# Optimization experiments

Hardware: AMD Instinct MI355X
Metric: run time of the kernel (lower is better)

The kernel has to match this reference:

```python
import jax, jax.numpy as jnp
import numpy as np

NUM_HEADS = 16


def setup_inputs() -> dict:
    key = jax.random.key(0)
    ks = jax.random.split(key, 5)
    B, N, D = 2, 2048, 1024
    scale = 1.0 / np.sqrt(D)  # roughly xavier-ish magnitude for weights
    return {
        "x": jax.random.normal(ks[0], (B, N, D), dtype=jnp.float32),
        "W_query": jax.random.normal(ks[1], (D, D), dtype=jnp.float32) * scale,
        "W_key": jax.random.normal(ks[2], (D, D), dtype=jnp.float32) * scale,
        "W_value": jax.random.normal(ks[3], (D, D), dtype=jnp.float32) * scale,
        "W_output": jax.random.normal(ks[4], (D, D), dtype=jnp.float32) * scale,
    }


def reference(x, W_query, W_key, W_value, W_output):
    # x: [B, N, D]; weights: [D, D]
    B, N, D = x.shape
    H = NUM_HEADS
    hd = D // H

    def mh_embed(W):
        # linear_embedding then split heads: [B, N, D] -> [B, H, N, hd]
        y = jnp.einsum("bnd,de->bne", x, W)
        return y.reshape(B, N, H, hd).transpose(0, 2, 1, 3)

    q = mh_embed(W_query)
    k = mh_embed(W_key)
    v = mh_embed(W_value)

    # NOTE: source scales by token_dim**-0.5 (full model dim), not head_dim
    attn = jnp.einsum("bhnd,bhmd->bhnm", q, k) * (D ** -0.5)
    attn = jax.nn.softmax(attn, axis=-1)
    out = jnp.einsum("bhnm,bhmd->bhnd", attn, v)  # [B, H, N, hd]

    out = out.transpose(0, 2, 1, 3).reshape(B, N, D)  # merge heads
    out = jnp.einsum("bnd,de->bne", out, W_output)
    return out
```

## Files before the change

### kernel.cpp

```cpp
#include <hip/hip_runtime.h>

#define D_MODEL 1024
#define N_TOK   2048
#define NHEAD   16
#define HDIM    64
#define BATCH   2
#define M_TOT   (BATCH*N_TOK)

typedef unsigned short u16;
typedef __bf16 bf16x8 __attribute__((ext_vector_type(8)));
typedef float  f32x4  __attribute__((ext_vector_type(4)));

#define QSCALE 0.04508422002777439f

__device__ __forceinline__ u16 f2bf(float f) {
  union { float f; unsigned u; } v; v.f = f;
  unsigned r = v.u + 0x7fffu + ((v.u >> 16) & 1u);
  return (u16)(r >> 16);
}

__device__ __forceinline__ float bf2f(u16 u) {
  union { unsigned u; float f; } v; v.u = ((unsigned)u) << 16; return v.f;
}

__device__ __forceinline__ unsigned pk2bf(float a, float b) {
#if __has_builtin(__builtin_amdgcn_cvt_pk_bf16_f32)
  typedef __bf16 bf16x2_t __attribute__((ext_vector_type(2)));
  bf16x2_t r = __builtin_amdgcn_cvt_pk_bf16_f32(a, b);
  union { bf16x2_t v; unsigned u; } c; c.v = r; return c.u;
#else
  return (unsigned)f2bf(a) | ((unsigned)f2bf(b) << 16);
#endif
}

__device__ __forceinline__ void gl2lds16(const void* g, void* l) {
  __builtin_amdgcn_global_load_lds(
      (__attribute__((address_space(1))) void*)g,
      (__attribute__((address_space(3))) void*)l, 16, 0, 0);
}

__global__ void prep_kernel(const float* __restrict__ x,
                            const float* __restrict__ s0, const float* __restrict__ s1,
                            const float* __restrict__ s2, const float* __restrict__ s3,
                            u16* __restrict__ xb,
                            u16* __restrict__ d0, u16* __restrict__ d1,
                            u16* __restrict__ d2, u16* __restrict__ d3) {
  const int t = threadIdx.y * 32 + threadIdx.x;
  if (blockIdx.z == 4) {
    int base = (blockIdx.y * 32 + blockIdx.x) * 256 + t;
#pragma unroll
    for (int r = 0; r < 4; ++r) {
      int i = base + r * 262144;
      float4 v = ((const float4*)x)[i];
      ushort4 o;
      o.x = f2bf(v.x); o.y = f2bf(v.y); o.z = f2bf(v.z); o.w = f2bf(v.w);
      ((ushort4*)xb)[i] = o;
    }
    return;
  }
  const float* src; u16* dst;
  switch (blockIdx.z) {
    case 0:  src = s0; dst = d0; break;
    case 1:  src = s1; dst = d1; break;
    case 2:  src = s2; dst = d2; break;
    default: src = s3; dst = d3; break;
  }
  float sc = (blockIdx.z == 0) ? QSCALE : 1.0f;
  __shared__ float tile[32][33];
  int xg = blockIdx.x * 32 + threadIdx.x;
  int ybase = blockIdx.y * 32;
#pragma unroll
  for (int r = 0; r < 4; ++r)
    tile[threadIdx.y + r*8][threadIdx.x] = src[(size_t)(ybase + threadIdx.y + r*8)*D_MODEL + xg];
  __syncthreads();
#pragma unroll
  for (int r = 0; r < 4; ++r)
    dst[(size_t)(blockIdx.x*32 + threadIdx.y + r*8)*D_MODEL + ybase + threadIdx.x] =
        f2bf(tile[threadIdx.x][threadIdx.y + r*8] * sc);
}

__device__ __forceinline__ void gemm_body(const u16* __restrict__ A,
                                          const u16* __restrict__ Bt,
                                          void* __restrict__ Cout, int mode) {
  __shared__ __attribute__((aligned(16))) u16 lA[2][128*32];
  __shared__ __attribute__((aligned(16))) u16 lB[2][128*32];
  const int t = threadIdx.x;
  const int lane = t & 63, w = t >> 6;
  const int wm = w >> 1, wn = w & 1;
  const int q4 = lane >> 4, l15 = lane & 15;
  const int m0 = blockIdx.y * 128, n0 = blockIdx.x * 128;

  const int c0 = t, c1 = 256 + t;
  const int r0 = c0 >> 2, g0 = (c0 & 3) ^ (r0 & 3);
  const int r1 = c1 >> 2, g1 = (c1 & 3) ^ (r1 & 3);

  f32x4 acc[4][4] = {};

  gl2lds16(A  + (size_t)(m0 + r0)*D_MODEL + g0*8, &lA[0][c0*8]);
  gl2lds16(Bt + (size_t)(n0 + r0)*D_MODEL + g0*8, &lB[0][c0*8]);
  gl2lds16(A  + (size_t)(m0 + r1)*D_MODEL + g1*8, &lA[0][c1*8]);
  gl2lds16(Bt + (size_t)(n0 + r1)*D_MODEL + g1*8, &lB[0][c1*8]);

  for (int it = 0; it < 32; ++it) {
    const int cur = it & 1;
    __syncthreads();
    if (it + 1 < 32) {
      const int kn = (it + 1) * 32;
      u16* dA = &lA[cur ^ 1][0]; u16* dB = &lB[cur ^ 1][0];
      gl2lds16(A  + (size_t)(m0 + r0)*D_MODEL + kn + g0*8, dA + c0*8);
      gl2lds16(Bt + (size_t)(n0 + r0)*D_MODEL + kn + g0*8, dB + c0*8);
      gl2lds16(A  + (size_t)(m0 + r1)*D_MODEL + kn + g1*8, dA + c1*8);
      gl2lds16(Bt + (size_t)(n0 + r1)*D_MODEL + kn + g1*8, dB + c1*8);
    }
    const u16* sA = &lA[cur][0]; const u16* sB = &lB[cur][0];
    bf16x8 af[4], bfr[4];
#pragma unroll
    for (int mi = 0; mi < 4; ++mi) {
      int r = wm*64 + mi*16 + l15;
      af[mi] = *(const bf16x8*)(sA + r*32 + ((q4 ^ (r & 3)) * 8));
    }
#pragma unroll
    for (int ni = 0; ni < 4; ++ni) {
      int r = wn*64 + ni*16 + l15;
      bfr[ni] = *(const bf16x8*)(sB + r*32 + ((q4 ^ (r & 3)) * 8));
    }
#pragma unroll
    for (int mi = 0; mi < 4; ++mi)
#pragma unroll
      for (int ni = 0; ni < 4; ++ni)
        acc[mi][ni] = __builtin_amdgcn_mfma_f32_16x16x32_bf16(af[mi], bfr[ni], acc[mi][ni], 0, 0, 0);
  }

#pragma unroll
  for (int mi = 0; mi < 4; ++mi) {
#pragma unroll
    for (int ni = 0; ni < 4; ++ni) {
      const int tok0 = m0 + wm*64 + mi*16 + q4*4;
      const int col  = n0 + wn*64 + ni*16 + l15;
      if (mode == 0) {
        u16* D = (u16*)Cout;
#pragma unroll
        for (int r = 0; r < 4; ++r) {
          int tok = tok0 + r;
          int b = tok >> 11, n = tok & (N_TOK-1);
          int h = col >> 6, d = col & (HDIM-1);
          D[(((size_t)(b*NHEAD + h))*N_TOK + n)*HDIM + d] = f2bf(acc[mi][ni][r]);
        }
      } else {
        int b = tok0 >> 11, n = tok0 & (N_TOK-1);
        int h = col >> 6, d = col & (HDIM-1);
        ushort4 pk;
        pk.x = f2bf(acc[mi][ni][0]); pk.y = f2bf(acc[mi][ni][1]);
        pk.z = f2bf(acc[mi][ni][2]); pk.w = f2bf(acc[mi][ni][3]);
        *(ushort4*)((u16*)Cout + ((size_t)(b*NHEAD + h)*HDIM + d)*N_TOK + n) = pk;
      }
    }
  }
}

__global__ __launch_bounds__(256) void qkv_kernel(const u16* __restrict__ xb,
    const u16* __restrict__ wqt, const u16* __restrict__ wkt, const u16* __restrict__ wvt,
    u16* __restrict__ Q, u16* __restrict__ K, u16* __restrict__ Vt) {
  int z = blockIdx.z;
  const u16* B = (z == 0) ? wqt : (z == 1) ? wkt : wvt;
  void* C = (z == 0) ? (void*)Q : (z == 1) ? (void*)K : (void*)Vt;
  gemm_body(xb, B, C, (z == 2) ? 2 : 0);
}

__global__ __launch_bounds__(256) void out_kernel(const u16* __restrict__ ctx,
    const u16* __restrict__ wot, float* __restrict__ out) {
  __shared__ __attribute__((aligned(16))) u16 lA[2][64*32];
  __shared__ __attribute__((aligned(16))) u16 lB[2][128*32];
  const int t = threadIdx.x;
  const int lane = t & 63, w = t >> 6;
  const int wm = w >> 1, wn = w & 1;
  const int q4 = lane >> 4, l15 = lane & 15;
  const int m0 = blockIdx.y * 64, n0 = blockIdx.x * 128;

  const int rA = t >> 2, gA = (t & 3) ^ (rA & 3);
  const int c0 = t, c1 = 256 + t;
  const int r0 = c0 >> 2, g0 = (c0 & 3) ^ (r0 & 3);
  const int r1 = c1 >> 2, g1 = (c1 & 3) ^ (r1 & 3);

  f32x4 acc[2][4] = {};

  gl2lds16(ctx + (size_t)(m0 + rA)*D_MODEL + gA*8, &lA[0][t*8]);
  gl2lds16(wot + (size_t)(n0 + r0)*D_MODEL + g0*8, &lB[0][c0*8]);
  gl2lds16(wot + (size_t)(n0 + r1)*D_MODEL + g1*8, &lB[0][c1*8]);

  for (int it = 0; it < 32; ++it) {
    const int cur = it & 1;
    __syncthreads();
    if (it + 1 < 32) {
      const int kn = (it + 1) * 32;
      u16* dA = &lA[cur ^ 1][0]; u16* dB = &lB[cur ^ 1][0];
      gl2lds16(ctx + (size_t)(m0 + rA)*D_MODEL + kn + gA*8, dA + t*8);
      gl2lds16(wot + (size_t)(n0 + r0)*D_MODEL + kn + g0*8, dB + c0*8);
      gl2lds16(wot + (size_t)(n0 + r1)*D_MODEL + kn + g1*8, dB + c1*8);
    }
    const u16* sA = &lA[cur][0]; const u16* sB = &lB[cur][0];
    bf16x8 af[2], bfr[4];
#pragma unroll
    for (int mi = 0; mi < 2; ++mi) {
      int r = wm*32 + mi*16 + l15;
      af[mi] = *(const bf16x8*)(sA + r*32 + ((q4 ^ (r & 3)) * 8));
    }
#pragma unroll
    for (int ni = 0; ni < 4; ++ni) {
      int r = wn*64 + ni*16 + l15;
      bfr[ni] = *(const bf16x8*)(sB + r*32 + ((q4 ^ (r & 3)) * 8));
    }
#pragma unroll
    for (int mi = 0; mi < 2; ++mi)
#pragma unroll
      for (int ni = 0; ni < 4; ++ni)
        acc[mi][ni] = __builtin_amdgcn_mfma_f32_16x16x32_bf16(af[mi], bfr[ni], acc[mi][ni], 0, 0, 0);
  }

#pragma unroll
  for (int mi = 0; mi < 2; ++mi) {
#pragma unroll
    for (int ni = 0; ni < 4; ++ni) {
      const int tok0 = m0 + wm*32 + mi*16 + q4*4;
      const int col  = n0 + wn*64 + ni*16 + l15;
#pragma unroll
      for (int r = 0; r < 4; ++r)
        out[(size_t)(tok0 + r)*D_MODEL + col] = acc[mi][ni][r];
    }
  }
}

__global__ __launch_bounds__(256, 3) void attn_kernel(const u16* __restrict__ Qg,
    const u16* __restrict__ Kg, const u16* __restrict__ Vtg,
    u16* __restrict__ Opart, float* __restrict__ Lpart) {
  __shared__ __attribute__((aligned(16))) u16 lds[24576];
  const int t = threadIdx.x;
  const int lane = t & 63, w = t >> 6;
  const int q4 = lane >> 4, l15 = lane & 15;
  const int bh = blockIdx.y;
  const int qb = blockIdx.x >> 1, half = blockIdx.x & 1;
  const int qw0 = qb * 128 + w * 32;
  const size_t kvBase = (size_t)bh * (N_TOK * HDIM);
  u16* myP = lds + 16384 + w * 2048;

  const int ck0 = t, ck1 = 256 + t;
  const int kr0 = ck0 >> 3, kg0 = (ck0 & 7) ^ (kr0 & 7);
  const int kr1 = ck1 >> 3, kg1 = (ck1 & 7) ^ (kr1 & 7);

  bf16x8 qf[2][2];
#pragma unroll
  for (int ni = 0; ni < 2; ++ni)
#pragma unroll
    for (int kk = 0; kk < 2; ++kk)
      qf[ni][kk] = *(const bf16x8*)(Qg + kvBase +
                    (size_t)(qw0 + ni*16 + l15)*HDIM + kk*32 + q4*8);

  f32x4 accO[4][2] = {};
  float lsum[2] = {0.f, 0.f};

  const int kvStart = half * 1024;
  gl2lds16(Kg  + kvBase + (size_t)(kvStart + kr0)*HDIM + kg0*8, lds + ck0*8);
  gl2lds16(Kg  + kvBase + (size_t)(kvStart + kr1)*HDIM + kg1*8, lds + ck1*8);
  gl2lds16(Vtg + kvBase + (size_t)kr0*N_TOK + kvStart + kg0*8,  lds + 8192 + ck0*8);
  gl2lds16(Vtg + kvBase + (size_t)kr1*N_TOK + kvStart + kg1*8,  lds + 8192 + ck1*8);

  for (int it = 0; it < 16; ++it) {
    const int cur = it & 1;
    __syncthreads();
    if (it + 1 < 16) {
      const int kvn = kvStart + (it + 1) * 64;
      u16* dK = lds + (cur ^ 1) * 4096;
      u16* dV = lds + 8192 + (cur ^ 1) * 4096;
      gl2lds16(Kg  + kvBase + (size_t)(kvn + kr0)*HDIM + kg0*8, dK + ck0*8);
      gl2lds16(Kg  + kvBase + (size_t)(kvn + kr1)*HDIM + kg1*8, dK + ck1*8);
      gl2lds16(Vtg + kvBase + (size_t)kr0*N_TOK + kvn + kg0*8,  dV + ck0*8);
      gl2lds16(Vtg + kvBase + (size_t)kr1*N_TOK + kvn + kg1*8,  dV + ck1*8);
    }
    const u16* sK = lds + cur * 4096;
    const u16* sV = lds + 8192 + cur * 4096;

#pragma unroll
    for (int mip = 0; mip < 4; ++mip) {
      const int kv = mip*16 + l15;
      f32x4 s[2] = {};
#pragma unroll
      for (int kk = 0; kk < 2; ++kk) {
        bf16x8 a = *(const bf16x8*)(sK + kv*64 + (((kk*4 + q4) ^ (l15 & 7)) * 8));
#pragma unroll
        for (int ni = 0; ni < 2; ++ni)
          s[ni] = __builtin_amdgcn_mfma_f32_16x16x32_bf16(a, qf[ni][kk], s[ni], 0, 0, 0);
      }
#pragma unroll
      for (int ni = 0; ni < 2; ++ni) {
        float p0 = __builtin_amdgcn_exp2f(s[ni][0]);
        float p1 = __builtin_amdgcn_exp2f(s[ni][1]);
        float p2 = __builtin_amdgcn_exp2f(s[ni][2]);
        float p3 = __builtin_amdgcn_exp2f(s[ni][3]);
        lsum[ni] += (p0 + p1) + (p2 + p3);
        uint2 u; u.x = pk2bf(p0, p1); u.y = pk2bf(p2, p3);
        const int qloc = ni*16 + l15;
        const int kv8 = mip*4 + q4;
        *(uint2*)(myP + qloc*64 + (((kv8 >> 1) ^ (qloc & 7)) * 8) + (kv8 & 1)*4) = u;
      }
    }

#pragma unroll
    for (int kk2 = 0; kk2 < 2; ++kk2) {
      bf16x8 bp[2];
#pragma unroll
      for (int ni = 0; ni < 2; ++ni)
        bp[ni] = *(const bf16x8*)(myP + (ni*16 + l15)*64 +
                                  (((kk2*4 + q4) ^ (l15 & 7)) * 8));
#pragma unroll
      for (int mi2 = 0; mi2 < 4; ++mi2) {
        const int d = mi2*16 + l15;
        bf16x8 av = *(const bf16x8*)(sV + d*64 + (((kk2*4 + q4) ^ (d & 7)) * 8));
#pragma unroll
        for (int ni = 0; ni < 2; ++ni)
          accO[mi2][ni] = __builtin_amdgcn_mfma_f32_16x16x32_bf16(av, bp[ni], accO[mi2][ni], 0, 0, 0);
      }
    }
  }

  const int b = bh >> 4, head = bh & (NHEAD-1);
  u16* Obase = Opart + (size_t)half * (M_TOT * D_MODEL);
#pragma unroll
  for (int ni = 0; ni < 2; ++ni) {
    float ls = lsum[ni];
    ls += __shfl_xor(ls, 16);
    ls += __shfl_xor(ls, 32);
    const int q = qw0 + ni*16 + l15;
    if (q4 == 0)
      Lpart[(size_t)half*(32*N_TOK) + bh*N_TOK + q] = ls;
    const size_t rb = ((size_t)(b*N_TOK + q))*D_MODEL + head*HDIM + q4*4;
#pragma unroll
    for (int mi2 = 0; mi2 < 4; ++mi2) {
      uint2 u;
      u.x = pk2bf(accO[mi2][ni][0], accO[mi2][ni][1]);
      u.y = pk2bf(accO[mi2][ni][2], accO[mi2][ni][3]);
      *(uint2*)(Obase + rb + mi2*16) = u;
    }
  }
}

__global__ __launch_bounds__(256) void combine_kernel(const u16* __restrict__ Opart,
    const float* __restrict__ Lpart, u16* __restrict__ ctx) {
  int i = blockIdx.x * 256 + threadIdx.x;
  int tok = i >> 7, c8 = i & 127;
  int n = tok & (N_TOK-1), b = tok >> 11;
  int h = c8 >> 3;
  int bh = b*NHEAD + h;
  float l = Lpart[(size_t)bh*N_TOK + n] + Lpart[(size_t)(32*N_TOK) + bh*N_TOK + n];
  float inv = 1.0f / l;
  const size_t off = (size_t)tok*D_MODEL + c8*8;
  ushort4 a0 = *(const ushort4*)(Opart + off);
  ushort4 a1 = *(const ushort4*)(Opart + off + 4);
  ushort4 b0 = *(const ushort4*)(Opart + (size_t)(M_TOT*D_MODEL) + off);
  ushort4 b1 = *(const ushort4*)(Opart + (size_t)(M_TOT*D_MODEL) + off + 4);
  uint2 o0, o1;
  o0.x = pk2bf((bf2f(a0.x)+bf2f(b0.x))*inv, (bf2f(a0.y)+bf2f(b0.y))*inv);
  o0.y = pk2bf((bf2f(a0.z)+bf2f(b0.z))*inv, (bf2f(a0.w)+bf2f(b0.w))*inv);
  o1.x = pk2bf((bf2f(a1.x)+bf2f(b1.x))*inv, (bf2f(a1.y)+bf2f(b1.y))*inv);
  o1.y = pk2bf((bf2f(a1.z)+bf2f(b1.z))*inv, (bf2f(a1.w)+bf2f(b1.w))*inv);
  *(uint2*)(ctx + off) = o0;
  *(uint2*)(ctx + off + 4) = o1;
}

extern "C" void kernel_launch(void* const* d_in, const int* in_sizes, int n_in,
                              void* d_out, int out_size, void* d_ws, size_t ws_size,
                              hipStream_t stream) {
  const float* x  = (const float*)d_in[0];
  const float* Wq = (const float*)d_in[1];
  const float* Wk = (const float*)d_in[2];
  const float* Wv = (const float*)d_in[3];
  const float* Wo = (const float*)d_in[4];
  float* out = (float*)d_out;

  char* ws = (char*)d_ws;
  u16* xb   = (u16*)(ws);
  u16* wqt  = (u16*)(ws + (8u  << 20));
  u16* wkt  = (u16*)(ws + (10u << 20));
  u16* wvt  = (u16*)(ws + (12u << 20));
  u16* wot  = (u16*)(ws + (14u << 20));
  u16* Qw   = (u16*)(ws + (16u << 20));
  u16* Kw   = (u16*)(ws + (24u << 20));
  u16* Vtw  = (u16*)(ws + (32u << 20));
  u16* ctx  = (u16*)(ws + (40u << 20));
  u16* Op   = (u16*)(ws + (48u << 20));
  float* Lp = (float*)(ws + (64u << 20));
  (void)in_sizes; (void)n_in; (void)out_size; (void)ws_size;

  prep_kernel<<<dim3(32, 32, 5), dim3(32, 8), 0, stream>>>(x, Wq, Wk, Wv, Wo,
                                                           xb, wqt, wkt, wvt, wot);
  qkv_kernel<<<dim3(8, 32, 3), 256, 0, stream>>>(xb, wqt, wkt, wvt, Qw, Kw, Vtw);
  attn_kernel<<<dim3(32, 32), 256, 0, stream>>>(Qw, Kw, Vtw, Op, Lp);
  combine_kernel<<<2048, 256, 0, stream>>>(Op, Lp, ctx);
  out_kernel<<<dim3(8, 64), 256, 0, stream>>>(ctx, wot, out);
}
```

Baseline: 201.5 us.

## Enlarge attention query tile per warp and split KV four ways

Each attention block now handles 256 queries (64 per warp) over a quarter of the KV sequence, instead of 128 queries over half. The goal is more MFMA reuse of every K/V tile staged in LDS. In exchange, the K/V double buffering is replaced by a single buffer with two barriers per step, so loads no longer overlap compute. Occupancy hints drop to 2 blocks, and the combine kernel now reads and sums four bf16 partials instead of two. The row-sum partials move to the start of the workspace, reusing the converted-input area.

```diff
diff --git a/kernel.cpp b/kernel.cpp
--- a/kernel.cpp
+++ b/kernel.cpp
@@ -230,7 +230,7 @@
   }
 }
 
-__global__ __launch_bounds__(256, 3) void attn_kernel(const u16* __restrict__ Qg,
+__global__ __launch_bounds__(256, 2) void attn_kernel(const u16* __restrict__ Qg,
     const u16* __restrict__ Kg, const u16* __restrict__ Vtg,
     u16* __restrict__ Opart, float* __restrict__ Lpart) {
   __shared__ __attribute__((aligned(16))) u16 lds[24576];
@@ -238,60 +238,49 @@
   const int lane = t & 63, w = t >> 6;
   const int q4 = lane >> 4, l15 = lane & 15;
   const int bh = blockIdx.y;
-  const int qb = blockIdx.x >> 1, half = blockIdx.x & 1;
-  const int qw0 = qb * 128 + w * 32;
+  const int qb = blockIdx.x >> 2, sp = blockIdx.x & 3;
+  const int qw0 = qb * 256 + w * 64;
   const size_t kvBase = (size_t)bh * (N_TOK * HDIM);
-  u16* myP = lds + 16384 + w * 2048;
+  u16* myP = lds + 8192 + w * 4096;
 
   const int ck0 = t, ck1 = 256 + t;
   const int kr0 = ck0 >> 3, kg0 = (ck0 & 7) ^ (kr0 & 7);
   const int kr1 = ck1 >> 3, kg1 = (ck1 & 7) ^ (kr1 & 7);
 
-  bf16x8 qf[2][2];
-#pragma unroll
-  for (int ni = 0; ni < 2; ++ni)
+  bf16x8 qf[4][2];
+#pragma unroll
+  for (int ni = 0; ni < 4; ++ni)
 #pragma unroll
     for (int kk = 0; kk < 2; ++kk)
       qf[ni][kk] = *(const bf16x8*)(Qg + kvBase +
                     (size_t)(qw0 + ni*16 + l15)*HDIM + kk*32 + q4*8);
 
-  f32x4 accO[4][2] = {};
-  float lsum[2] = {0.f, 0.f};
-
-  const int kvStart = half * 1024;
-  gl2lds16(Kg  + kvBase + (size_t)(kvStart + kr0)*HDIM + kg0*8, lds + ck0*8);
-  gl2lds16(Kg  + kvBase + (size_t)(kvStart + kr1)*HDIM + kg1*8, lds + ck1*8);
-  gl2lds16(Vtg + kvBase + (size_t)kr0*N_TOK + kvStart + kg0*8,  lds + 8192 + ck0*8);
-  gl2lds16(Vtg + kvBase + (size_t)kr1*N_TOK + kvStart + kg1*8,  lds + 8192 + ck1*8);
-
-  for (int it = 0; it < 16; ++it) {
-    const int cur = it & 1;
+  f32x4 accO[4][4] = {};
+  float lsum[4] = {0.f, 0.f, 0.f, 0.f};
+
+  const int kvStart = sp * 512;
+  for (int it = 0; it < 8; ++it) {
+    const int kv0 = kvStart + it * 64;
     __syncthreads();
-    if (it + 1 < 16) {
-      const int kvn = kvStart + (it + 1) * 64;
-      u16* dK = lds + (cur ^ 1) * 4096;
-      u16* dV = lds + 8192 + (cur ^ 1) * 4096;
-      gl2lds16(Kg  + kvBase + (size_t)(kvn + kr0)*HDIM + kg0*8, dK + ck0*8);
-      gl2lds16(Kg  + kvBase + (size_t)(kvn + kr1)*HDIM + kg1*8, dK + ck1*8);
-      gl2lds16(Vtg + kvBase + (size_t)kr0*N_TOK + kvn + kg0*8,  dV + ck0*8);
-      gl2lds16(Vtg + kvBase + (size_t)kr1*N_TOK + kvn + kg1*8,  dV + ck1*8);
-    }
-    const u16* sK = lds + cur * 4096;
-    const u16* sV = lds + 8192 + cur * 4096;
+    gl2lds16(Kg  + kvBase + (size_t)(kv0 + kr0)*HDIM + kg0*8, lds + ck0*8);
+    gl2lds16(Kg  + kvBase + (size_t)(kv0 + kr1)*HDIM + kg1*8, lds + ck1*8);
+    gl2lds16(Vtg + kvBase + (size_t)kr0*N_TOK + kv0 + kg0*8,  lds + 4096 + ck0*8);
+    gl2lds16(Vtg + kvBase + (size_t)kr1*N_TOK + kv0 + kg1*8,  lds + 4096 + ck1*8);
+    __syncthreads();
 
 #pragma unroll
     for (int mip = 0; mip < 4; ++mip) {
       const int kv = mip*16 + l15;
-      f32x4 s[2] = {};
+      f32x4 s[4] = {};
 #pragma unroll
       for (int kk = 0; kk < 2; ++kk) {
-        bf16x8 a = *(const bf16x8*)(sK + kv*64 + (((kk*4 + q4) ^ (l15 & 7)) * 8));
-#pragma unroll
-        for (int ni = 0; ni < 2; ++ni)
+        bf16x8 a = *(const bf16x8*)(lds + kv*64 + (((kk*4 + q4) ^ (l15 & 7)) * 8));
+#pragma unroll
+        for (int ni = 0; ni < 4; ++ni)
           s[ni] = __builtin_amdgcn_mfma_f32_16x16x32_bf16(a, qf[ni][kk], s[ni], 0, 0, 0);
       }
 #pragma unroll
-      for (int ni = 0; ni < 2; ++ni) {
+      for (int ni = 0; ni < 4; ++ni) {
         float p0 = __builtin_amdgcn_exp2f(s[ni][0]);
         float p1 = __builtin_amdgcn_exp2f(s[ni][1]);
         float p2 = __builtin_amdgcn_exp2f(s[ni][2]);
@@ -306,32 +295,33 @@
 
 #pragma unroll
     for (int kk2 = 0; kk2 < 2; ++kk2) {
-      bf16x8 bp[2];
-#pragma unroll
-      for (int ni = 0; ni < 2; ++ni)
+      bf16x8 bp[4];
+#pragma unroll
+      for (int ni = 0; ni < 4; ++ni)
         bp[ni] = *(const bf16x8*)(myP + (ni*16 + l15)*64 +
                                   (((kk2*4 + q4) ^ (l15 & 7)) * 8));
 #pragma unroll
       for (int mi2 = 0; mi2 < 4; ++mi2) {
         const int d = mi2*16 + l15;
-        bf16x8 av = *(const bf16x8*)(sV + d*64 + (((kk2*4 + q4) ^ (d & 7)) * 8));
-#pragma unroll
-        for (int ni = 0; ni < 2; ++ni)
+        bf16x8 av = *(const bf16x8*)(lds + 4096 + d*64 +
+                                     (((kk2*4 + q4) ^ (d & 7)) * 8));
+#pragma unroll
+        for (int ni = 0; ni < 4; ++ni)
           accO[mi2][ni] = __builtin_amdgcn_mfma_f32_16x16x32_bf16(av, bp[ni], accO[mi2][ni], 0, 0, 0);
       }
     }
   }
 
   const int b = bh >> 4, head = bh & (NHEAD-1);
-  u16* Obase = Opart + (size_t)half * (M_TOT * D_MODEL);
-#pragma unroll
-  for (int ni = 0; ni < 2; ++ni) {
+  u16* Obase = Opart + (size_t)sp * (M_TOT * D_MODEL);
+#pragma unroll
+  for (int ni = 0; ni < 4; ++ni) {
     float ls = lsum[ni];
     ls += __shfl_xor(ls, 16);
     ls += __shfl_xor(ls, 32);
     const int q = qw0 + ni*16 + l15;
     if (q4 == 0)
-      Lpart[(size_t)half*(32*N_TOK) + bh*N_TOK + q] = ls;
+      Lpart[(size_t)sp*(32*N_TOK) + bh*N_TOK + q] = ls;
     const size_t rb = ((size_t)(b*N_TOK + q))*D_MODEL + head*HDIM + q4*4;
 #pragma unroll
     for (int mi2 = 0; mi2 < 4; ++mi2) {
@@ -350,18 +340,28 @@
   int n = tok & (N_TOK-1), b = tok >> 11;
   int h = c8 >> 3;
   int bh = b*NHEAD + h;
-  float l = Lpart[(size_t)bh*N_TOK + n] + Lpart[(size_t)(32*N_TOK) + bh*N_TOK + n];
+  float l = 0.f;
+#pragma unroll
+  for (int s = 0; s < 4; ++s)
+    l += Lpart[(size_t)s*(32*N_TOK) + bh*N_TOK + n];
   float inv = 1.0f / l;
   const size_t off = (size_t)tok*D_MODEL + c8*8;
-  ushort4 a0 = *(const ushort4*)(Opart + off);
-  ushort4 a1 = *(const ushort4*)(Opart + off + 4);
-  ushort4 b0 = *(const ushort4*)(Opart + (size_t)(M_TOT*D_MODEL) + off);
-  ushort4 b1 = *(const ushort4*)(Opart + (size_t)(M_TOT*D_MODEL) + off + 4);
+  float acc[8] = {};
+#pragma unroll
+  for (int s = 0; s < 4; ++s) {
+    const u16* base = Opart + (size_t)s*(M_TOT*D_MODEL) + off;
+    ushort4 a0 = *(const ushort4*)(base);
+    ushort4 a1 = *(const ushort4*)(base + 4);
+    acc[0] += bf2f(a0.x); acc[1] += bf2f(a0.y);
+    acc[2] += bf2f(a0.z); acc[3] += bf2f(a0.w);
+    acc[4] += bf2f(a1.x); acc[5] += bf2f(a1.y);
+    acc[6] += bf2f(a1.z); acc[7] += bf2f(a1.w);
+  }
   uint2 o0, o1;
-  o0.x = pk2bf((bf2f(a0.x)+bf2f(b0.x))*inv, (bf2f(a0.y)+bf2f(b0.y))*inv);
-  o0.y = pk2bf((bf2f(a0.z)+bf2f(b0.z))*inv, (bf2f(a0.w)+bf2f(b0.w))*inv);
-  o1.x = pk2bf((bf2f(a1.x)+bf2f(b1.x))*inv, (bf2f(a1.y)+bf2f(b1.y))*inv);
-  o1.y = pk2bf((bf2f(a1.z)+bf2f(b1.z))*inv, (bf2f(a1.w)+bf2f(b1.w))*inv);
+  o0.x = pk2bf(acc[0]*inv, acc[1]*inv);
+  o0.y = pk2bf(acc[2]*inv, acc[3]*inv);
+  o1.x = pk2bf(acc[4]*inv, acc[5]*inv);
+  o1.y = pk2bf(acc[6]*inv, acc[7]*inv);
   *(uint2*)(ctx + off) = o0;
   *(uint2*)(ctx + off + 4) = o1;
 }
@@ -387,7 +387,7 @@
   u16* Vtw  = (u16*)(ws + (32u << 20));
   u16* ctx  = (u16*)(ws + (40u << 20));
   u16* Op   = (u16*)(ws + (48u << 20));
-  float* Lp = (float*)(ws + (64u << 20));
+  float* Lp = (float*)(ws);
   (void)in_sizes; (void)n_in; (void)out_size; (void)ws_size;
 
   prep_kernel<<<dim3(32, 32, 5), dim3(32, 8), 0, stream>>>(x, Wq, Wk, Wv, Wo,
```

Measured after the change: 207.9 us. 1.03x slower.

## Fuse split-KV combine into output projection and single-buffer attention LDS

Applied to the files above, without the earlier changes.

Removes the separate combine kernel: the output-projection GEMM now loads both partial attention outputs and their row sums, normalizes them in registers, and writes the combined bf16 tile into shared memory while the weight tile streams in asynchronously. This drops one launch and a round trip of the context tensor through global memory, at the cost of register-path loads for the A operand instead of direct-to-LDS copies. Separately, the attention kernel goes from double-buffered to single-buffered K/V staging with two barriers per step. That shrinks shared memory so the occupancy hint can rise from 3 to 4 blocks, trading away load/compute overlap. The row-sum buffer is moved to the start of the workspace, reusing the x bf16 region, which is no longer needed by that point.

```diff
diff --git a/kernel.cpp b/kernel.cpp
--- a/kernel.cpp
+++ b/kernel.cpp
@@ -31,6 +31,12 @@
 #else
   return (unsigned)f2bf(a) | ((unsigned)f2bf(b) << 16);
 #endif
+}
+
+__device__ __forceinline__ unsigned comb2(unsigned a, unsigned b, float inv) {
+  float x = (bf2f((u16)(a & 0xffff)) + bf2f((u16)(b & 0xffff))) * inv;
+  float y = (bf2f((u16)(a >> 16))   + bf2f((u16)(b >> 16)))   * inv;
+  return pk2bf(x, y);
 }
 
 __device__ __forceinline__ void gl2lds16(const void* g, void* l) {
@@ -167,8 +173,9 @@
   gemm_body(xb, B, C, (z == 2) ? 2 : 0);
 }
 
-__global__ __launch_bounds__(256) void out_kernel(const u16* __restrict__ ctx,
-    const u16* __restrict__ wot, float* __restrict__ out) {
+__global__ __launch_bounds__(256) void out_kernel(const u16* __restrict__ Op,
+    const float* __restrict__ Lp, const u16* __restrict__ wot,
+    float* __restrict__ out) {
   __shared__ __attribute__((aligned(16))) u16 lA[2][64*32];
   __shared__ __attribute__((aligned(16))) u16 lB[2][128*32];
   const int t = threadIdx.x;
@@ -178,23 +185,44 @@
   const int m0 = blockIdx.y * 64, n0 = blockIdx.x * 128;
 
   const int rA = t >> 2, gA = (t & 3) ^ (rA & 3);
+  const int tok = m0 + rA;
+  const int nA = tok & (N_TOK-1), bA = tok >> 11;
   const int c0 = t, c1 = 256 + t;
   const int r0 = c0 >> 2, g0 = (c0 & 3) ^ (r0 & 3);
   const int r1 = c1 >> 2, g1 = (c1 & 3) ^ (r1 & 3);
 
   f32x4 acc[2][4] = {};
-
-  gl2lds16(ctx + (size_t)(m0 + rA)*D_MODEL + gA*8, &lA[0][t*8]);
-  gl2lds16(wot + (size_t)(n0 + r0)*D_MODEL + g0*8, &lB[0][c0*8]);
-  gl2lds16(wot + (size_t)(n0 + r1)*D_MODEL + g1*8, &lB[0][c1*8]);
+  uint4 pa, pb;
+  float l0, l1;
+
+  {
+    const size_t off = (size_t)tok*D_MODEL + gA*8;
+    pa = *(const uint4*)(Op + off);
+    pb = *(const uint4*)(Op + (size_t)(M_TOT*D_MODEL) + off);
+    l0 = Lp[(size_t)(bA*NHEAD)*N_TOK + nA];
+    l1 = Lp[(size_t)(32*N_TOK) + (size_t)(bA*NHEAD)*N_TOK + nA];
+    gl2lds16(wot + (size_t)(n0 + r0)*D_MODEL + g0*8, &lB[0][c0*8]);
+    gl2lds16(wot + (size_t)(n0 + r1)*D_MODEL + g1*8, &lB[0][c1*8]);
+    float inv = 1.0f / (l0 + l1);
+    uint4 o;
+    o.x = comb2(pa.x, pb.x, inv); o.y = comb2(pa.y, pb.y, inv);
+    o.z = comb2(pa.z, pb.z, inv); o.w = comb2(pa.w, pb.w, inv);
+    *(uint4*)(&lA[0][t*8]) = o;
+  }
 
   for (int it = 0; it < 32; ++it) {
     const int cur = it & 1;
     __syncthreads();
-    if (it + 1 < 32) {
+    const bool hasNext = (it + 1) < 32;
+    if (hasNext) {
       const int kn = (it + 1) * 32;
-      u16* dA = &lA[cur ^ 1][0]; u16* dB = &lB[cur ^ 1][0];
-      gl2lds16(ctx + (size_t)(m0 + rA)*D_MODEL + kn + gA*8, dA + t*8);
+      const int h2 = (it + 1) >> 1;
+      const size_t off = (size_t)tok*D_MODEL + kn + gA*8;
+      pa = *(const uint4*)(Op + off);
+      pb = *(const uint4*)(Op + (size_t)(M_TOT*D_MODEL) + off);
+      l0 = Lp[(size_t)(bA*NHEAD + h2)*N_TOK + nA];
+      l1 = Lp[(size_t)(32*N_TOK) + (size_t)(bA*NHEAD + h2)*N_TOK + nA];
+      u16* dB = &lB[cur ^ 1][0];
       gl2lds16(wot + (size_t)(n0 + r0)*D_MODEL + kn + g0*8, dB + c0*8);
       gl2lds16(wot + (size_t)(n0 + r1)*D_MODEL + kn + g1*8, dB + c1*8);
     }
@@ -215,6 +243,13 @@
 #pragma unroll
       for (int ni = 0; ni < 4; ++ni)
         acc[mi][ni] = __builtin_amdgcn_mfma_f32_16x16x32_bf16(af[mi], bfr[ni], acc[mi][ni], 0, 0, 0);
+    if (hasNext) {
+      float inv = 1.0f / (l0 + l1);
+      uint4 o;
+      o.x = comb2(pa.x, pb.x, inv); o.y = comb2(pa.y, pb.y, inv);
+      o.z = comb2(pa.z, pb.z, inv); o.w = comb2(pa.w, pb.w, inv);
+      *(uint4*)(&lA[cur ^ 1][t*8]) = o;
+    }
   }
 
 #pragma unroll
@@ -230,18 +265,18 @@
   }
 }
 
-__global__ __launch_bounds__(256, 3) void attn_kernel(const u16* __restrict__ Qg,
+__global__ __launch_bounds__(256, 4) void attn_kernel(const u16* __restrict__ Qg,
     const u16* __restrict__ Kg, const u16* __restrict__ Vtg,
     u16* __restrict__ Opart, float* __restrict__ Lpart) {
-  __shared__ __attribute__((aligned(16))) u16 lds[24576];
+  __shared__ __attribute__((aligned(16))) u16 lds[16384];
   const int t = threadIdx.x;
   const int lane = t & 63, w = t >> 6;
   const int q4 = lane >> 4, l15 = lane & 15;
   const int bh = blockIdx.y;
-  const int qb = blockIdx.x >> 1, half = blockIdx.x & 1;
+  const int qb = blockIdx.x >> 1, sp = blockIdx.x & 1;
   const int qw0 = qb * 128 + w * 32;
   const size_t kvBase = (size_t)bh * (N_TOK * HDIM);
-  u16* myP = lds + 16384 + w * 2048;
+  u16* myP = lds + 8192 + w * 2048;
 
   const int ck0 = t, ck1 = 256 + t;
   const int kr0 = ck0 >> 3, kg0 = (ck0 & 7) ^ (kr0 & 7);
@@ -258,26 +293,15 @@
   f32x4 accO[4][2] = {};
   float lsum[2] = {0.f, 0.f};
 
-  const int kvStart = half * 1024;
-  gl2lds16(Kg  + kvBase + (size_t)(kvStart + kr0)*HDIM + kg0*8, lds + ck0*8);
-  gl2lds16(Kg  + kvBase + (size_t)(kvStart + kr1)*HDIM + kg1*8, lds + ck1*8);
-  gl2lds16(Vtg + kvBase + (size_t)kr0*N_TOK + kvStart + kg0*8,  lds + 8192 + ck0*8);
-  gl2lds16(Vtg + kvBase + (size_t)kr1*N_TOK + kvStart + kg1*8,  lds + 8192 + ck1*8);
-
+  const int kvStart = sp * 1024;
   for (int it = 0; it < 16; ++it) {
-    const int cur = it & 1;
+    const int kv0 = kvStart + it * 64;
     __syncthreads();
-    if (it + 1 < 16) {
-      const int kvn = kvStart + (it + 1) * 64;
-      u16* dK = lds + (cur ^ 1) * 4096;
-      u16* dV = lds + 8192 + (cur ^ 1) * 4096;
-      gl2lds16(Kg  + kvBase + (size_t)(kvn + kr0)*HDIM + kg0*8, dK + ck0*8);
-      gl2lds16(Kg  + kvBase + (size_t)(kvn + kr1)*HDIM + kg1*8, dK + ck1*8);
-      gl2lds16(Vtg + kvBase + (size_t)kr0*N_TOK + kvn + kg0*8,  dV + ck0*8);
-      gl2lds16(Vtg + kvBase + (size_t)kr1*N_TOK + kvn + kg1*8,  dV + ck1*8);
-    }
-    const u16* sK = lds + cur * 4096;
-    const u16* sV = lds + 8192 + cur * 4096;
+    gl2lds16(Kg  + kvBase + (size_t)(kv0 + kr0)*HDIM + kg0*8, lds + ck0*8);
+    gl2lds16(Kg  + kvBase + (size_t)(kv0 + kr1)*HDIM + kg1*8, lds + ck1*8);
+    gl2lds16(Vtg + kvBase + (size_t)kr0*N_TOK + kv0 + kg0*8,  lds + 4096 + ck0*8);
+    gl2lds16(Vtg + kvBase + (size_t)kr1*N_TOK + kv0 + kg1*8,  lds + 4096 + ck1*8);
+    __syncthreads();
 
 #pragma unroll
     for (int mip = 0; mip < 4; ++mip) {
@@ -285,7 +309,7 @@
       f32x4 s[2] = {};
 #pragma unroll
       for (int kk = 0; kk < 2; ++kk) {
-        bf16x8 a = *(const bf16x8*)(sK + kv*64 + (((kk*4 + q4) ^ (l15 & 7)) * 8));
+        bf16x8 a = *(const bf16x8*)(lds + kv*64 + (((kk*4 + q4) ^ (l15 & 7)) * 8));
 #pragma unroll
         for (int ni = 0; ni < 2; ++ni)
           s[ni] = __builtin_amdgcn_mfma_f32_16x16x32_bf16(a, qf[ni][kk], s[ni], 0, 0, 0);
@@ -314,7 +338,8 @@
 #pragma unroll
       for (int mi2 = 0; mi2 < 4; ++mi2) {
         const int d = mi2*16 + l15;
-        bf16x8 av = *(const bf16x8*)(sV + d*64 + (((kk2*4 + q4) ^ (d & 7)) * 8));
+        bf16x8 av = *(const bf16x8*)(lds + 4096 + d*64 +
+                                     (((kk2*4 + q4) ^ (d & 7)) * 8));
 #pragma unroll
         for (int ni = 0; ni < 2; ++ni)
           accO[mi2][ni] = __builtin_amdgcn_mfma_f32_16x16x32_bf16(av, bp[ni], accO[mi2][ni], 0, 0, 0);
@@ -323,7 +348,7 @@
   }
 
   const int b = bh >> 4, head = bh & (NHEAD-1);
-  u16* Obase = Opart + (size_t)half * (M_TOT * D_MODEL);
+  u16* Obase = Opart + (size_t)sp * (M_TOT * D_MODEL);
 #pragma unroll
   for (int ni = 0; ni < 2; ++ni) {
     float ls = lsum[ni];
@@ -331,7 +356,7 @@
     ls += __shfl_xor(ls, 32);
     const int q = qw0 + ni*16 + l15;
     if (q4 == 0)
-      Lpart[(size_t)half*(32*N_TOK) + bh*N_TOK + q] = ls;
+      Lpart[(size_t)sp*(32*N_TOK) + bh*N_TOK + q] = ls;
     const size_t rb = ((size_t)(b*N_TOK + q))*D_MODEL + head*HDIM + q4*4;
 #pragma unroll
     for (int mi2 = 0; mi2 < 4; ++mi2) {
@@ -341,29 +366,6 @@
       *(uint2*)(Obase + rb + mi2*16) = u;
     }
   }
-}
-
-__global__ __launch_bounds__(256) void combine_kernel(const u16* __restrict__ Opart,
-    const float* __restrict__ Lpart, u16* __restrict__ ctx) {
-  int i = blockIdx.x * 256 + threadIdx.x;
-  int tok = i >> 7, c8 = i & 127;
-  int n = tok & (N_TOK-1), b = tok >> 11;
-  int h = c8 >> 3;
-  int bh = b*NHEAD + h;
-  float l = Lpart[(size_t)bh*N_TOK + n] + Lpart[(size_t)(32*N_TOK) + bh*N_TOK + n];
-  float inv = 1.0f / l;
-  const size_t off = (size_t)tok*D_MODEL + c8*8;
-  ushort4 a0 = *(const ushort4*)(Opart + off);
-  ushort4 a1 = *(const ushort4*)(Opart + off + 4);
-  ushort4 b0 = *(const ushort4*)(Opart + (size_t)(M_TOT*D_MODEL) + off);
-  ushort4 b1 = *(const ushort4*)(Opart + (size_t)(M_TOT*D_MODEL) + off + 4);
-  uint2 o0, o1;
-  o0.x = pk2bf((bf2f(a0.x)+bf2f(b0.x))*inv, (bf2f(a0.y)+bf2f(b0.y))*inv);
-  o0.y = pk2bf((bf2f(a0.z)+bf2f(b0.z))*inv, (bf2f(a0.w)+bf2f(b0.w))*inv);
-  o1.x = pk2bf((bf2f(a1.x)+bf2f(b1.x))*inv, (bf2f(a1.y)+bf2f(b1.y))*inv);
-  o1.y = pk2bf((bf2f(a1.z)+bf2f(b1.z))*inv, (bf2f(a1.w)+bf2f(b1.w))*inv);
-  *(uint2*)(ctx + off) = o0;
-  *(uint2*)(ctx + off + 4) = o1;
 }
 
 extern "C" void kernel_launch(void* const* d_in, const int* in_sizes, int n_in,
@@ -385,15 +387,13 @@
   u16* Qw   = (u16*)(ws + (16u << 20));
   u16* Kw   = (u16*)(ws + (24u << 20));
   u16* Vtw  = (u16*)(ws + (32u << 20));
-  u16* ctx  = (u16*)(ws + (40u << 20));
-  u16* Op   = (u16*)(ws + (48u << 20));
-  float* Lp = (float*)(ws + (64u << 20));
+  u16* Op   = (u16*)(ws + (40u << 20));
+  float* Lp = (float*)(ws);
   (void)in_sizes; (void)n_in; (void)out_size; (void)ws_size;
 
   prep_kernel<<<dim3(32, 32, 5), dim3(32, 8), 0, stream>>>(x, Wq, Wk, Wv, Wo,
                                                            xb, wqt, wkt, wvt, wot);
   qkv_kernel<<<dim3(8, 32, 3), 256, 0, stream>>>(xb, wqt, wkt, wvt, Qw, Kw, Vtw);
   attn_kernel<<<dim3(32, 32), 256, 0, stream>>>(Qw, Kw, Vtw, Op, Lp);
-  combine_kernel<<<2048, 256, 0, stream>>>(Op, Lp, ctx);
-  out_kernel<<<dim3(8, 64), 256, 0, stream>>>(ctx, wot, out);
-}
+  out_kernel<<<dim3(8, 64), 256, 0, stream>>>(Op, Lp, wot, out);
+}
```

Measured after the change: 207.1 us. 1.03x slower.
